# Performance work log

Measured on AMD Instinct MI355X. Metric: run time of the kernel, lower is better.

Reference implementation:

```python
import jax, jax.numpy as jnp
import numpy as np
import math

HIDDEN = 1024
HEADS = 16
HEAD_DIM = HIDDEN // HEADS
B, S = 4, 2048


def setup_inputs() -> dict:
    key = jax.random.key(0)
    ks = jax.random.split(key, 10)
    x = jax.random.normal(ks[0], (B, S, HIDDEN), dtype=jnp.float32)
    time_intervals = jax.random.uniform(ks[1], (B, S, S), dtype=jnp.float32)
    mask = jax.random.randint(ks[2], (B, 1, S, S), 0, 2, dtype=jnp.int32)
    scale = 1.0 / math.sqrt(HIDDEN)
    Wq = jax.random.normal(ks[3], (HIDDEN, HIDDEN), dtype=jnp.float32) * scale
    bq = jnp.zeros((HIDDEN,), dtype=jnp.float32)
    Wk = jax.random.normal(ks[4], (HIDDEN, HIDDEN), dtype=jnp.float32) * scale
    bk = jnp.zeros((HIDDEN,), dtype=jnp.float32)
    Wv = jax.random.normal(ks[5], (HIDDEN, HIDDEN), dtype=jnp.float32) * scale
    bv = jnp.zeros((HIDDEN,), dtype=jnp.float32)
    alpha = jnp.asarray(0.1, dtype=jnp.float32)
    return {"x": x, "time_intervals": time_intervals, "mask": mask,
            "Wq": Wq, "bq": bq, "Wk": Wk, "bk": bk, "Wv": Wv, "bv": bv,
            "alpha": alpha}


def reference(x, time_intervals, mask, Wq, bq, Wk, bk, Wv, bv, alpha):
    b, s, _ = x.shape
    # projections -> [b, heads, s, head_dim]
    def proj(W, bias):
        y = x @ W + bias
        return y.reshape(b, s, HEADS, HEAD_DIM).transpose(0, 2, 1, 3)
    Q = proj(Wq, bq)
    K = proj(Wk, bk)
    V = proj(Wv, bv)
    scores = jnp.einsum('bhqd,bhkd->bhqk', Q, K) / math.sqrt(HEAD_DIM)
    # additive time-decay bias, broadcast over heads
    scores = scores + (-jnp.abs(alpha)) * time_intervals[:, None, :, :]
    scores = jnp.where(mask == 0, jnp.float32(-1e9), scores)
    attn = jax.nn.softmax(scores, axis=-1)
    out = jnp.einsum('bhqk,bhkd->bhqd', attn, V)
    return out.transpose(0, 2, 1, 3).reshape(b, s, HIDDEN)
```

## Files before the change

kernel.cpp:

```cpp
#include <hip/hip_runtime.h>
#include <hip/hip_bf16.h>
#include <hip/hip_fp16.h>

#define BATCH 4
#define SEQ   2048
#define HID   1024
#define HEADS 16
#define HDIM  64
#define MROWS (BATCH * SEQ)
#define LOG2E 1.4426950408889634f
#define SCL   (LOG2E / 8.0f)

typedef _Float16 v8h __attribute__((ext_vector_type(8)));
typedef _Float16 v4h __attribute__((ext_vector_type(4)));
typedef _Float16 v2h __attribute__((ext_vector_type(2)));
typedef float    v4f __attribute__((ext_vector_type(4)));
typedef int      v4i __attribute__((ext_vector_type(4)));

#define MFMA16(a, b, c) __builtin_amdgcn_mfma_f32_16x16x32_f16((a), (b), (c), 0, 0, 0)
#define MFMA16K16(a, b, c) __builtin_amdgcn_mfma_f32_16x16x16f16((a), (b), (c), 0, 0, 0)

__device__ inline int pk2(float a, float b) {
    return __builtin_bit_cast(int, __builtin_amdgcn_cvt_pkrtz(a, b));
}

__device__ __forceinline__ void async16(const void* g, void* l) {
    __builtin_amdgcn_global_load_lds(
        (const __attribute__((address_space(1))) unsigned int*)g,
        (__attribute__((address_space(3))) unsigned int*)l, 16, 0, 0);
}

#define SWZ(row, chunk) (((row) * 64) + ((((chunk) ^ ((row) & 7))) * 8))

__global__ __launch_bounds__(256) void prep(
    const float* __restrict__ x, _Float16* __restrict__ xb,
    const float* __restrict__ W0, const float* __restrict__ W1,
    const float* __restrict__ W2, _Float16* __restrict__ Wt) {
    __shared__ float t[32][33];
    const int bid = blockIdx.x;
    const int tid = threadIdx.x;
    if (bid < 4096) {
        int i = bid * 256 + tid;
        const float4* xp = (const float4*)x;
        float4 a = xp[2 * i];
        float4 b = xp[2 * i + 1];
        v4i o;
        o[0] = pk2(a.x, a.y); o[1] = pk2(a.z, a.w);
        o[2] = pk2(b.x, b.y); o[3] = pk2(b.z, b.w);
        ((v4i*)xb)[i] = o;
    } else {
        int tt = bid - 4096;
        int z = tt >> 10;
        int rem = tt & 1023;
        const float* W = (z == 0) ? W0 : (z == 1 ? W1 : W2);
        _Float16* dst = Wt + (size_t)z * HID * HID;
        int bx = (rem & 31) * 32, by = (rem >> 5) * 32;
        int tx = tid & 31, ty = tid >> 5;
#pragma unroll
        for (int i = 0; i < 4; i++)
            t[ty + i * 8][tx] = W[(size_t)(by + ty + i * 8) * HID + bx + tx];
        __syncthreads();
#pragma unroll
        for (int i = 0; i < 4; i++)
            dst[(size_t)(bx + ty + i * 8) * HID + by + tx] = (_Float16)t[tx][ty + i * 8];
    }
}

__global__ __launch_bounds__(256) void gemm_bias(
    const _Float16* __restrict__ xb, const _Float16* __restrict__ wt,
    const float* __restrict__ bq, const float* __restrict__ bk,
    const float* __restrict__ bv,
    _Float16* __restrict__ Qb, _Float16* __restrict__ Kb, _Float16* __restrict__ Vtb,
    const float* __restrict__ tiv, const int* __restrict__ msk,
    const float* __restrict__ alphap, _Float16* __restrict__ biasT) {
    __shared__ _Float16 smem[2 * 2 * 128 * 64];
    const int bid = blockIdx.x;
    const int tid = threadIdx.x;

    if (bid < 1536) {
        const int nid = (bid & 7) * 192 + (bid >> 3);
        const int mode = nid >> 9;
        const int within = nid & 511;
        const int n0 = (within & 7) * 128;
        const int m0 = (within >> 3) * 128;
        const _Float16* w = wt + (size_t)mode * HID * HID;
        _Float16 (*As)[128 * 64] = (_Float16(*)[128 * 64])smem;
        _Float16 (*Bs)[128 * 64] = (_Float16(*)[128 * 64])(smem + 2 * 128 * 64);
        const int wv = tid >> 6, lane = tid & 63;
        const int quad = lane >> 4, l15 = lane & 15;
        const int wr = wv >> 1, wc = wv & 1;

        v4f acc[4][4];
#pragma unroll
        for (int i = 0; i < 4; i++)
#pragma unroll
            for (int j = 0; j < 4; j++) acc[i][j] = (v4f){0.f, 0.f, 0.f, 0.f};

        const int srow = lane >> 3;
        const int schk = lane & 7;
        const _Float16* Ag = xb + (size_t)m0 * HID;
        const _Float16* Bg = w + (size_t)n0 * HID;

#define STAGEG(buf_, k0_)                                                   \
        {                                                                   \
            _Pragma("unroll")                                               \
            for (int i_ = 0; i_ < 4; i_++) {                                \
                int ra_ = wv * 32 + i_ * 8 + srow;                          \
                int ca_ = schk ^ (ra_ & 7);                                 \
                async16(Ag + (size_t)ra_ * HID + (k0_) + ca_ * 8,           \
                        &As[buf_][(wv * 32 + i_ * 8) * 64]);                \
                async16(Bg + (size_t)ra_ * HID + (k0_) + ca_ * 8,           \
                        &Bs[buf_][(wv * 32 + i_ * 8) * 64]);                \
            }                                                               \
        }

        STAGEG(0, 0)
        __syncthreads();

        for (int it = 0; it < HID / 64; it++) {
            const int cur = it & 1;
            if (it + 1 < HID / 64) STAGEG(cur ^ 1, (it + 1) * 64)
#pragma unroll
            for (int kc = 0; kc < 2; kc++) {
                v8h af[4], bf[4];
#pragma unroll
                for (int t = 0; t < 4; t++) {
                    af[t] = *(const v8h*)&As[cur][SWZ(wr * 64 + t * 16 + l15, kc * 4 + quad)];
                    bf[t] = *(const v8h*)&Bs[cur][SWZ(wc * 64 + t * 16 + l15, kc * 4 + quad)];
                }
#pragma unroll
                for (int tm = 0; tm < 4; tm++)
#pragma unroll
                    for (int tn = 0; tn < 4; tn++)
                        acc[tm][tn] = MFMA16(af[tm], bf[tn], acc[tm][tn]);
            }
            __syncthreads();
        }
#undef STAGEG

        const float* pb = (mode == 0) ? bq : (mode == 1 ? bk : bv);
        const float oscl = (mode == 0) ? SCL : 1.0f;
#pragma unroll
        for (int tm = 0; tm < 4; tm++) {
#pragma unroll
            for (int tn = 0; tn < 4; tn++) {
                int n = n0 + wc * 64 + tn * 16 + l15;
                float bval = pb[n];
                int h = n >> 6, d = n & 63;
#pragma unroll
                for (int r = 0; r < 4; r++) {
                    int m = m0 + wr * 64 + tm * 16 + quad * 4 + r;
                    int b = m >> 11, s = m & 2047;
                    _Float16 hv = (_Float16)((acc[tm][tn][r] + bval) * oscl);
                    if (mode == 2) {
                        Vtb[(((size_t)(b * HEADS + h) * HDIM + d) * SEQ) + s] = hv;
                    } else {
                        _Float16* dst = (mode == 0) ? Qb : Kb;
                        dst[((size_t)(b * HEADS + h) * SEQ + s) * HDIM + d] = hv;
                    }
                }
            }
        }
    } else {
        const int t = bid - 1536;
        const int kc0 = (t & 7) * 256;
        const int Q16 = (t >> 3) & 127;
        const int b = t >> 10;
        _Float16* L = smem;
        const float ca = -fabsf(alphap[0]) * LOG2E;
        const int prow = tid >> 6;
        const int pcol = (tid & 63) * 4;
#pragma unroll
        for (int pi = 0; pi < 4; pi++) {
            int r = pi * 4 + prow;
            size_t g = ((size_t)b * SEQ + Q16 * 16 + r) * SEQ + kc0 + pcol;
            float4 tv = *(const float4*)(tiv + g);
            int4   mv = *(const int4*)(msk + g);
            float f0 = mv.x ? ca * tv.x : -57344.0f;
            float f1 = mv.y ? ca * tv.y : -57344.0f;
            float f2 = mv.z ? ca * tv.z : -57344.0f;
            float f3 = mv.w ? ca * tv.w : -57344.0f;
            int2 o; o.x = pk2(f0, f1); o.y = pk2(f2, f3);
            *(int2*)&L[r * 264 + pcol] = o;
        }
        __syncthreads();
        const int lane = tid & 63, tq = tid >> 6;
#pragma unroll
        for (int it = 0; it < 4; it++) {
            int K16i = it * 4 + tq;
            int kl = K16i * 16 + (lane >> 4) * 4;
            int qr = lane & 15;
            int2 v = *(const int2*)&L[qr * 264 + kl];
            size_t o = ((((size_t)b * 128 + (kc0 >> 4) + K16i) * 128 + Q16) * 64 + lane) * 4;
            *(int2*)&biasT[o] = v;
        }
    }
}

__global__ __launch_bounds__(256, 4) void attn(
    const _Float16* __restrict__ Qb, const _Float16* __restrict__ Kb,
    const _Float16* __restrict__ Vtb, const _Float16* __restrict__ biasT,
    float* __restrict__ out) {
    const int wg  = (blockIdx.y << 4) | blockIdx.x;
    const int nid = ((wg & 7) << 7) | (wg >> 3);
    const int bh = nid >> 4;
    const int qt = nid & 15;
    const int b = bh >> 4, h = bh & 15;
    const int tid = threadIdx.x;
    const int wv = tid >> 6, lane = tid & 63;
    const int quad = lane >> 4, l15 = lane & 15;

    __shared__ _Float16 Ks[2][64 * 64];
    __shared__ _Float16 Vs[2][64 * 64];

    const int q0 = qt * 128 + wv * 32;
    const int Q16a = q0 >> 4;

    const _Float16* Qp = Qb + (size_t)(b * HEADS + h) * SEQ * HDIM;
    const _Float16* Kp = Kb + (size_t)(b * HEADS + h) * SEQ * HDIM;
    const _Float16* Vp = Vtb + (size_t)(b * HEADS + h) * HDIM * SEQ;
    const _Float16* Bbase = biasT + (size_t)b * 128 * 128 * 64 * 4;

    v8h qf[2][2];
#pragma unroll
    for (int tm = 0; tm < 2; tm++)
#pragma unroll
        for (int kc = 0; kc < 2; kc++)
            qf[tm][kc] = *(const v8h*)&Qp[(size_t)(q0 + tm * 16 + l15) * HDIM + kc * 32 + quad * 8];

    v4f oacc[2][4];
#pragma unroll
    for (int i = 0; i < 2; i++)
#pragma unroll
        for (int j = 0; j < 4; j++) oacc[i][j] = (v4f){0.f, 0.f, 0.f, 0.f};
    float lsum[2] = {0.f, 0.f};

    const int srow = lane >> 3, schk = lane & 7;

#define STAGE(buf_, key0_)                                                  \
    {                                                                       \
        _Pragma("unroll")                                                   \
        for (int i_ = 0; i_ < 2; i_++) {                                    \
            int r_ = wv * 16 + i_ * 8 + srow;                               \
            int c_ = schk ^ (r_ & 7);                                       \
            async16(Kp + (size_t)((key0_) + r_) * HDIM + c_ * 8,            \
                    &Ks[buf_][(wv * 16 + i_ * 8) * 64]);                    \
            async16(Vp + (size_t)r_ * SEQ + (key0_) + c_ * 8,               \
                    &Vs[buf_][(wv * 16 + i_ * 8) * 64]);                    \
        }                                                                   \
    }

#define BLOAD(key0_)                                                        \
    {                                                                       \
        _Pragma("unroll")                                                   \
        for (int nt_ = 0; nt_ < 4; nt_++)                                   \
            _Pragma("unroll")                                               \
            for (int tm_ = 0; tm_ < 2; tm_++)                               \
                bl[nt_][tm_] = *(const int2*)&Bbase[((((size_t)((key0_) >> 4) + nt_) * 128 + Q16a + tm_) * 64 + lane) * 4]; \
    }

    int2 bl[4][2];
    STAGE(0, 0)
    BLOAD(0)
    __syncthreads();

    for (int kt = 0; kt < SEQ / 64; kt++) {
        const int cur = kt & 1;
        const int key0 = kt * 64;

        v4f sacc[4][2];
#pragma unroll
        for (int nt = 0; nt < 4; nt++)
#pragma unroll
            for (int tm = 0; tm < 2; tm++) {
                v4h bv = __builtin_bit_cast(v4h, bl[nt][tm]);
                sacc[nt][tm] = (v4f){(float)bv[0], (float)bv[1], (float)bv[2], (float)bv[3]};
            }

        if (kt + 1 < SEQ / 64) {
            STAGE(cur ^ 1, key0 + 64)
            BLOAD(key0 + 64)
        }

#pragma unroll
        for (int kc = 0; kc < 2; kc++) {
            v8h kfr[4];
#pragma unroll
            for (int nt = 0; nt < 4; nt++)
                kfr[nt] = *(const v8h*)&Ks[cur][SWZ(nt * 16 + l15, kc * 4 + quad)];
#pragma unroll
            for (int nt = 0; nt < 4; nt++)
#pragma unroll
                for (int tm = 0; tm < 2; tm++)
                    sacc[nt][tm] = MFMA16(kfr[nt], qf[tm][kc], sacc[nt][tm]);
        }

        int2 pfr[4][2];
#pragma unroll
        for (int nt = 0; nt < 4; nt++)
#pragma unroll
            for (int tm = 0; tm < 2; tm++) {
                float p0 = __builtin_amdgcn_exp2f(sacc[nt][tm][0]);
                float p1 = __builtin_amdgcn_exp2f(sacc[nt][tm][1]);
                float p2 = __builtin_amdgcn_exp2f(sacc[nt][tm][2]);
                float p3 = __builtin_amdgcn_exp2f(sacc[nt][tm][3]);
                int2 pkv;
                pkv.x = pk2(p0, p1);
                pkv.y = pk2(p2, p3);
                lsum[tm] += (p0 + p1) + (p2 + p3);
                pfr[nt][tm] = pkv;
            }

#pragma unroll
        for (int g = 0; g < 4; g++) {
            v4h vfr[4];
#pragma unroll
            for (int nt = 0; nt < 4; nt++) {
                int row = nt * 16 + l15;
                int cc = g * 2 + (quad >> 1);
                vfr[nt] = *(const v4h*)&Vs[cur][row * 64 + ((cc ^ (row & 7)) * 8) + (quad & 1) * 4];
            }
#pragma unroll
            for (int tm = 0; tm < 2; tm++) {
                v4h pa = __builtin_bit_cast(v4h, pfr[g][tm]);
#pragma unroll
                for (int nt = 0; nt < 4; nt++)
                    oacc[tm][nt] = MFMA16K16(pa, vfr[nt], oacc[tm][nt]);
            }
        }

        __syncthreads();
    }

#undef STAGE
#undef BLOAD

#pragma unroll
    for (int tm = 0; tm < 2; tm++) {
        float lt = lsum[tm];
        lt += __shfl_xor(lt, 16);
        lt += __shfl_xor(lt, 32);
        float inv[4];
#pragma unroll
        for (int r = 0; r < 4; r++)
            inv[r] = 1.0f / __shfl(lt, quad * 4 + r);
#pragma unroll
        for (int nt = 0; nt < 4; nt++)
#pragma unroll
            for (int r = 0; r < 4; r++) {
                int q = q0 + tm * 16 + quad * 4 + r;
                int d = nt * 16 + l15;
                out[((size_t)b * SEQ + q) * HID + h * HDIM + d] = oacc[tm][nt][r] * inv[r];
            }
    }
}

extern "C" void kernel_launch(void* const* d_in, const int* in_sizes, int n_in,
                              void* d_out, int out_size, void* d_ws, size_t ws_size,
                              hipStream_t stream) {
    const float* x    = (const float*)d_in[0];
    const float* tiv  = (const float*)d_in[1];
    const int*   msk  = (const int*)d_in[2];
    const float* Wq   = (const float*)d_in[3];
    const float* bq   = (const float*)d_in[4];
    const float* Wk   = (const float*)d_in[5];
    const float* bk   = (const float*)d_in[6];
    const float* Wv   = (const float*)d_in[7];
    const float* bv   = (const float*)d_in[8];
    const float* alp  = (const float*)d_in[9];

    char* ws = (char*)d_ws;
    const size_t XB_OFF = 0;
    const size_t WT_OFF = XB_OFF + (size_t)MROWS * HID * 2;
    const size_t Q_OFF  = WT_OFF + (size_t)3 * HID * HID * 2;
    const size_t K_OFF  = Q_OFF + (size_t)MROWS * HID * 2;
    const size_t V_OFF  = K_OFF + (size_t)MROWS * HID * 2;
    const size_t B_OFF  = V_OFF + (size_t)MROWS * HID * 2;

    _Float16* xb   = (_Float16*)(ws + XB_OFF);
    _Float16* wt   = (_Float16*)(ws + WT_OFF);
    _Float16* Qb   = (_Float16*)(ws + Q_OFF);
    _Float16* Kb   = (_Float16*)(ws + K_OFF);
    _Float16* Vtb  = (_Float16*)(ws + V_OFF);
    _Float16* bias = (_Float16*)(ws + B_OFF);

    prep<<<4096 + 3072, 256, 0, stream>>>(x, xb, Wq, Wk, Wv, wt);
    gemm_bias<<<1536 + 4096, 256, 0, stream>>>(xb, wt, bq, bk, bv, Qb, Kb, Vtb,
                                               tiv, msk, alp, bias);
    attn<<<dim3(SEQ / 128, BATCH * HEADS), 256, 0, stream>>>(Qb, Kb, Vtb, bias,
                                                             (float*)d_out);
}
```

Baseline: 364.5 us.

## Fuse time-decay and mask bias into attention, drop precomputed bias tensor

Removes the pass in the projection kernel that turned time_intervals and mask into a pre-laid-out fp16 bias tensor. The attention kernel now loads the fp32 intervals and int32 mask directly per tile and builds the additive bias in registers, saving one launch phase and a 32MB intermediate write and read. In exchange every head re-reads the 8-byte-per-element raw inputs, so traffic grows a lot unless the caches absorb the reuse across the 16 heads, and the larger register footprint lowers attention occupancy from 4 to 3 blocks. The prep kernel also becomes a 256-block persistent loop processing 28 units per block.

```diff
diff --git a/kernel.cpp b/kernel.cpp
--- a/kernel.cpp
+++ b/kernel.cpp
@@ -39,168 +39,136 @@
     __shared__ float t[32][33];
     const int bid = blockIdx.x;
     const int tid = threadIdx.x;
-    if (bid < 4096) {
-        int i = bid * 256 + tid;
-        const float4* xp = (const float4*)x;
-        float4 a = xp[2 * i];
-        float4 b = xp[2 * i + 1];
-        v4i o;
-        o[0] = pk2(a.x, a.y); o[1] = pk2(a.z, a.w);
-        o[2] = pk2(b.x, b.y); o[3] = pk2(b.z, b.w);
-        ((v4i*)xb)[i] = o;
-    } else {
-        int tt = bid - 4096;
-        int z = tt >> 10;
-        int rem = tt & 1023;
-        const float* W = (z == 0) ? W0 : (z == 1 ? W1 : W2);
-        _Float16* dst = Wt + (size_t)z * HID * HID;
-        int bx = (rem & 31) * 32, by = (rem >> 5) * 32;
-        int tx = tid & 31, ty = tid >> 5;
-#pragma unroll
-        for (int i = 0; i < 4; i++)
-            t[ty + i * 8][tx] = W[(size_t)(by + ty + i * 8) * HID + bx + tx];
-        __syncthreads();
-#pragma unroll
-        for (int i = 0; i < 4; i++)
-            dst[(size_t)(bx + ty + i * 8) * HID + by + tx] = (_Float16)t[tx][ty + i * 8];
-    }
-}
-
-__global__ __launch_bounds__(256) void gemm_bias(
+    for (int u = 0; u < 28; u++) {
+        const int unit = bid * 28 + u;
+        if (unit < 4096) {
+            int i = unit * 256 + tid;
+            const float4* xp = (const float4*)x;
+            float4 a = xp[2 * i];
+            float4 b = xp[2 * i + 1];
+            v4i o;
+            o[0] = pk2(a.x, a.y); o[1] = pk2(a.z, a.w);
+            o[2] = pk2(b.x, b.y); o[3] = pk2(b.z, b.w);
+            ((v4i*)xb)[i] = o;
+        } else {
+            int tt = unit - 4096;
+            int z = tt >> 10;
+            int rem = tt & 1023;
+            const float* W = (z == 0) ? W0 : (z == 1 ? W1 : W2);
+            _Float16* dst = Wt + (size_t)z * HID * HID;
+            int bx = (rem & 31) * 32, by = (rem >> 5) * 32;
+            int tx = tid & 31, ty = tid >> 5;
+#pragma unroll
+            for (int i = 0; i < 4; i++)
+                t[ty + i * 8][tx] = W[(size_t)(by + ty + i * 8) * HID + bx + tx];
+            __syncthreads();
+#pragma unroll
+            for (int i = 0; i < 4; i++)
+                dst[(size_t)(bx + ty + i * 8) * HID + by + tx] = (_Float16)t[tx][ty + i * 8];
+            __syncthreads();
+        }
+    }
+}
+
+__global__ __launch_bounds__(256) void gemm_qkv(
     const _Float16* __restrict__ xb, const _Float16* __restrict__ wt,
     const float* __restrict__ bq, const float* __restrict__ bk,
     const float* __restrict__ bv,
-    _Float16* __restrict__ Qb, _Float16* __restrict__ Kb, _Float16* __restrict__ Vtb,
-    const float* __restrict__ tiv, const int* __restrict__ msk,
-    const float* __restrict__ alphap, _Float16* __restrict__ biasT) {
+    _Float16* __restrict__ Qb, _Float16* __restrict__ Kb, _Float16* __restrict__ Vtb) {
     __shared__ _Float16 smem[2 * 2 * 128 * 64];
     const int bid = blockIdx.x;
     const int tid = threadIdx.x;
 
-    if (bid < 1536) {
-        const int nid = (bid & 7) * 192 + (bid >> 3);
-        const int mode = nid >> 9;
-        const int within = nid & 511;
-        const int n0 = (within & 7) * 128;
-        const int m0 = (within >> 3) * 128;
-        const _Float16* w = wt + (size_t)mode * HID * HID;
-        _Float16 (*As)[128 * 64] = (_Float16(*)[128 * 64])smem;
-        _Float16 (*Bs)[128 * 64] = (_Float16(*)[128 * 64])(smem + 2 * 128 * 64);
-        const int wv = tid >> 6, lane = tid & 63;
-        const int quad = lane >> 4, l15 = lane & 15;
-        const int wr = wv >> 1, wc = wv & 1;
-
-        v4f acc[4][4];
-#pragma unroll
-        for (int i = 0; i < 4; i++)
-#pragma unroll
-            for (int j = 0; j < 4; j++) acc[i][j] = (v4f){0.f, 0.f, 0.f, 0.f};
-
-        const int srow = lane >> 3;
-        const int schk = lane & 7;
-        const _Float16* Ag = xb + (size_t)m0 * HID;
-        const _Float16* Bg = w + (size_t)n0 * HID;
+    const int nid = (bid & 7) * 192 + (bid >> 3);
+    const int mode = nid >> 9;
+    const int within = nid & 511;
+    const int n0 = (within & 7) * 128;
+    const int m0 = (within >> 3) * 128;
+    const _Float16* w = wt + (size_t)mode * HID * HID;
+    _Float16 (*As)[128 * 64] = (_Float16(*)[128 * 64])smem;
+    _Float16 (*Bs)[128 * 64] = (_Float16(*)[128 * 64])(smem + 2 * 128 * 64);
+    const int wv = tid >> 6, lane = tid & 63;
+    const int quad = lane >> 4, l15 = lane & 15;
+    const int wr = wv >> 1, wc = wv & 1;
+
+    v4f acc[4][4];
+#pragma unroll
+    for (int i = 0; i < 4; i++)
+#pragma unroll
+        for (int j = 0; j < 4; j++) acc[i][j] = (v4f){0.f, 0.f, 0.f, 0.f};
+
+    const int srow = lane >> 3;
+    const int schk = lane & 7;
+    const _Float16* Ag = xb + (size_t)m0 * HID;
+    const _Float16* Bg = w + (size_t)n0 * HID;
 
 #define STAGEG(buf_, k0_)                                                   \
-        {                                                                   \
-            _Pragma("unroll")                                               \
-            for (int i_ = 0; i_ < 4; i_++) {                                \
-                int ra_ = wv * 32 + i_ * 8 + srow;                          \
-                int ca_ = schk ^ (ra_ & 7);                                 \
-                async16(Ag + (size_t)ra_ * HID + (k0_) + ca_ * 8,           \
-                        &As[buf_][(wv * 32 + i_ * 8) * 64]);                \
-                async16(Bg + (size_t)ra_ * HID + (k0_) + ca_ * 8,           \
-                        &Bs[buf_][(wv * 32 + i_ * 8) * 64]);                \
-            }                                                               \
-        }
-
-        STAGEG(0, 0)
+    {                                                                       \
+        _Pragma("unroll")                                                   \
+        for (int i_ = 0; i_ < 4; i_++) {                                    \
+            int ra_ = wv * 32 + i_ * 8 + srow;                              \
+            int ca_ = schk ^ (ra_ & 7);                                     \
+            async16(Ag + (size_t)ra_ * HID + (k0_) + ca_ * 8,               \
+                    &As[buf_][(wv * 32 + i_ * 8) * 64]);                    \
+            async16(Bg + (size_t)ra_ * HID + (k0_) + ca_ * 8,               \
+                    &Bs[buf_][(wv * 32 + i_ * 8) * 64]);                    \
+        }                                                                   \
+    }
+
+    STAGEG(0, 0)
+    __syncthreads();
+
+    for (int it = 0; it < HID / 64; it++) {
+        const int cur = it & 1;
+        if (it + 1 < HID / 64) STAGEG(cur ^ 1, (it + 1) * 64)
+#pragma unroll
+        for (int kc = 0; kc < 2; kc++) {
+            v8h af[4], bf[4];
+#pragma unroll
+            for (int t = 0; t < 4; t++) {
+                af[t] = *(const v8h*)&As[cur][SWZ(wr * 64 + t * 16 + l15, kc * 4 + quad)];
+                bf[t] = *(const v8h*)&Bs[cur][SWZ(wc * 64 + t * 16 + l15, kc * 4 + quad)];
+            }
+#pragma unroll
+            for (int tm = 0; tm < 4; tm++)
+#pragma unroll
+                for (int tn = 0; tn < 4; tn++)
+                    acc[tm][tn] = MFMA16(af[tm], bf[tn], acc[tm][tn]);
+        }
         __syncthreads();
-
-        for (int it = 0; it < HID / 64; it++) {
-            const int cur = it & 1;
-            if (it + 1 < HID / 64) STAGEG(cur ^ 1, (it + 1) * 64)
-#pragma unroll
-            for (int kc = 0; kc < 2; kc++) {
-                v8h af[4], bf[4];
-#pragma unroll
-                for (int t = 0; t < 4; t++) {
-                    af[t] = *(const v8h*)&As[cur][SWZ(wr * 64 + t * 16 + l15, kc * 4 + quad)];
-                    bf[t] = *(const v8h*)&Bs[cur][SWZ(wc * 64 + t * 16 + l15, kc * 4 + quad)];
+    }
+#undef STAGEG
+
+    const float* pb = (mode == 0) ? bq : (mode == 1 ? bk : bv);
+    const float oscl = (mode == 0) ? SCL : 1.0f;
+#pragma unroll
+    for (int tm = 0; tm < 4; tm++) {
+#pragma unroll
+        for (int tn = 0; tn < 4; tn++) {
+            int n = n0 + wc * 64 + tn * 16 + l15;
+            float bval = pb[n];
+            int h = n >> 6, d = n & 63;
+#pragma unroll
+            for (int r = 0; r < 4; r++) {
+                int m = m0 + wr * 64 + tm * 16 + quad * 4 + r;
+                int b = m >> 11, s = m & 2047;
+                _Float16 hv = (_Float16)((acc[tm][tn][r] + bval) * oscl);
+                if (mode == 2) {
+                    Vtb[(((size_t)(b * HEADS + h) * HDIM + d) * SEQ) + s] = hv;
+                } else {
+                    _Float16* dst = (mode == 0) ? Qb : Kb;
+                    dst[((size_t)(b * HEADS + h) * SEQ + s) * HDIM + d] = hv;
                 }
-#pragma unroll
-                for (int tm = 0; tm < 4; tm++)
-#pragma unroll
-                    for (int tn = 0; tn < 4; tn++)
-                        acc[tm][tn] = MFMA16(af[tm], bf[tn], acc[tm][tn]);
-            }
-            __syncthreads();
-        }
-#undef STAGEG
-
-        const float* pb = (mode == 0) ? bq : (mode == 1 ? bk : bv);
-        const float oscl = (mode == 0) ? SCL : 1.0f;
-#pragma unroll
-        for (int tm = 0; tm < 4; tm++) {
-#pragma unroll
-            for (int tn = 0; tn < 4; tn++) {
-                int n = n0 + wc * 64 + tn * 16 + l15;
-                float bval = pb[n];
-                int h = n >> 6, d = n & 63;
-#pragma unroll
-                for (int r = 0; r < 4; r++) {
-                    int m = m0 + wr * 64 + tm * 16 + quad * 4 + r;
-                    int b = m >> 11, s = m & 2047;
-                    _Float16 hv = (_Float16)((acc[tm][tn][r] + bval) * oscl);
-                    if (mode == 2) {
-                        Vtb[(((size_t)(b * HEADS + h) * HDIM + d) * SEQ) + s] = hv;
-                    } else {
-                        _Float16* dst = (mode == 0) ? Qb : Kb;
-                        dst[((size_t)(b * HEADS + h) * SEQ + s) * HDIM + d] = hv;
-                    }
-                }
-            }
-        }
-    } else {
-        const int t = bid - 1536;
-        const int kc0 = (t & 7) * 256;
-        const int Q16 = (t >> 3) & 127;
-        const int b = t >> 10;
-        _Float16* L = smem;
-        const float ca = -fabsf(alphap[0]) * LOG2E;
-        const int prow = tid >> 6;
-        const int pcol = (tid & 63) * 4;
-#pragma unroll
-        for (int pi = 0; pi < 4; pi++) {
-            int r = pi * 4 + prow;
-            size_t g = ((size_t)b * SEQ + Q16 * 16 + r) * SEQ + kc0 + pcol;
-            float4 tv = *(const float4*)(tiv + g);
-            int4   mv = *(const int4*)(msk + g);
-            float f0 = mv.x ? ca * tv.x : -57344.0f;
-            float f1 = mv.y ? ca * tv.y : -57344.0f;
-            float f2 = mv.z ? ca * tv.z : -57344.0f;
-            float f3 = mv.w ? ca * tv.w : -57344.0f;
-            int2 o; o.x = pk2(f0, f1); o.y = pk2(f2, f3);
-            *(int2*)&L[r * 264 + pcol] = o;
-        }
-        __syncthreads();
-        const int lane = tid & 63, tq = tid >> 6;
-#pragma unroll
-        for (int it = 0; it < 4; it++) {
-            int K16i = it * 4 + tq;
-            int kl = K16i * 16 + (lane >> 4) * 4;
-            int qr = lane & 15;
-            int2 v = *(const int2*)&L[qr * 264 + kl];
-            size_t o = ((((size_t)b * 128 + (kc0 >> 4) + K16i) * 128 + Q16) * 64 + lane) * 4;
-            *(int2*)&biasT[o] = v;
-        }
-    }
-}
-
-__global__ __launch_bounds__(256, 4) void attn(
+            }
+        }
+    }
+}
+
+__global__ __launch_bounds__(256, 3) void attn(
     const _Float16* __restrict__ Qb, const _Float16* __restrict__ Kb,
-    const _Float16* __restrict__ Vtb, const _Float16* __restrict__ biasT,
-    float* __restrict__ out) {
+    const _Float16* __restrict__ Vtb,
+    const float* __restrict__ tiv, const int* __restrict__ msk,
+    const float* __restrict__ alphap, float* __restrict__ out) {
     const int wg  = (blockIdx.y << 4) | blockIdx.x;
     const int nid = ((wg & 7) << 7) | (wg >> 3);
     const int bh = nid >> 4;
@@ -214,12 +182,16 @@
     __shared__ _Float16 Vs[2][64 * 64];
 
     const int q0 = qt * 128 + wv * 32;
-    const int Q16a = q0 >> 4;
+    const float ca = -fabsf(alphap[0]) * LOG2E;
 
     const _Float16* Qp = Qb + (size_t)(b * HEADS + h) * SEQ * HDIM;
     const _Float16* Kp = Kb + (size_t)(b * HEADS + h) * SEQ * HDIM;
     const _Float16* Vp = Vtb + (size_t)(b * HEADS + h) * HDIM * SEQ;
-    const _Float16* Bbase = biasT + (size_t)b * 128 * 128 * 64 * 4;
+
+    size_t rowb[2];
+#pragma unroll
+    for (int tm = 0; tm < 2; tm++)
+        rowb[tm] = ((size_t)b * SEQ + q0 + tm * 16 + l15) * SEQ + quad * 4;
 
     v8h qf[2][2];
 #pragma unroll
@@ -250,18 +222,22 @@
         }                                                                   \
     }
 
-#define BLOAD(key0_)                                                        \
+#define TLOAD(key0_)                                                        \
     {                                                                       \
         _Pragma("unroll")                                                   \
         for (int nt_ = 0; nt_ < 4; nt_++)                                   \
             _Pragma("unroll")                                               \
-            for (int tm_ = 0; tm_ < 2; tm_++)                               \
-                bl[nt_][tm_] = *(const int2*)&Bbase[((((size_t)((key0_) >> 4) + nt_) * 128 + Q16a + tm_) * 64 + lane) * 4]; \
-    }
-
-    int2 bl[4][2];
+            for (int tm_ = 0; tm_ < 2; tm_++) {                             \
+                size_t g_ = rowb[tm_] + (key0_) + nt_ * 16;                 \
+                tvl[nt_][tm_] = *(const float4*)(tiv + g_);                 \
+                mvl[nt_][tm_] = *(const int4*)(msk + g_);                   \
+            }                                                               \
+    }
+
+    float4 tvl[4][2];
+    int4   mvl[4][2];
     STAGE(0, 0)
-    BLOAD(0)
+    TLOAD(0)
     __syncthreads();
 
     for (int kt = 0; kt < SEQ / 64; kt++) {
@@ -273,13 +249,17 @@
         for (int nt = 0; nt < 4; nt++)
 #pragma unroll
             for (int tm = 0; tm < 2; tm++) {
-                v4h bv = __builtin_bit_cast(v4h, bl[nt][tm]);
-                sacc[nt][tm] = (v4f){(float)bv[0], (float)bv[1], (float)bv[2], (float)bv[3]};
+                v4f s;
+                s[0] = mvl[nt][tm].x ? ca * tvl[nt][tm].x : -57344.0f;
+                s[1] = mvl[nt][tm].y ? ca * tvl[nt][tm].y : -57344.0f;
+                s[2] = mvl[nt][tm].z ? ca * tvl[nt][tm].z : -57344.0f;
+                s[3] = mvl[nt][tm].w ? ca * tvl[nt][tm].w : -57344.0f;
+                sacc[nt][tm] = s;
             }
 
         if (kt + 1 < SEQ / 64) {
             STAGE(cur ^ 1, key0 + 64)
-            BLOAD(key0 + 64)
+            TLOAD(key0 + 64)
         }
 
 #pragma unroll
@@ -333,7 +313,7 @@
     }
 
 #undef STAGE
-#undef BLOAD
+#undef TLOAD
 
 #pragma unroll
     for (int tm = 0; tm < 2; tm++) {
@@ -375,18 +355,16 @@
     const size_t Q_OFF  = WT_OFF + (size_t)3 * HID * HID * 2;
     const size_t K_OFF  = Q_OFF + (size_t)MROWS * HID * 2;
     const size_t V_OFF  = K_OFF + (size_t)MROWS * HID * 2;
-    const size_t B_OFF  = V_OFF + (size_t)MROWS * HID * 2;
 
     _Float16* xb   = (_Float16*)(ws + XB_OFF);
     _Float16* wt   = (_Float16*)(ws + WT_OFF);
     _Float16* Qb   = (_Float16*)(ws + Q_OFF);
     _Float16* Kb   = (_Float16*)(ws + K_OFF);
     _Float16* Vtb  = (_Float16*)(ws + V_OFF);
-    _Float16* bias = (_Float16*)(ws + B_OFF);
-
-    prep<<<4096 + 3072, 256, 0, stream>>>(x, xb, Wq, Wk, Wv, wt);
-    gemm_bias<<<1536 + 4096, 256, 0, stream>>>(xb, wt, bq, bk, bv, Qb, Kb, Vtb,
-                                               tiv, msk, alp, bias);
-    attn<<<dim3(SEQ / 128, BATCH * HEADS), 256, 0, stream>>>(Qb, Kb, Vtb, bias,
+
+    prep<<<256, 256, 0, stream>>>(x, xb, Wq, Wk, Wv, wt);
+    gemm_qkv<<<1536, 256, 0, stream>>>(xb, wt, bq, bk, bv, Qb, Kb, Vtb);
+    attn<<<dim3(SEQ / 128, BATCH * HEADS), 256, 0, stream>>>(Qb, Kb, Vtb,
+                                                             tiv, msk, alp,
                                                              (float*)d_out);
 }
```

Result: slower. 587.4 us (+61.2%).
